# Kernel optimization log

Hardware: AMD Instinct MI355X
Metric: run time of the kernel (lower is better)

Reference implementation:

```python
import math
import jax, jax.numpy as jnp
import numpy as np

L, B, D, Z, H, N = 2048, 8, 1024, 128, 2048, 16
MAXPOS = 2048
LAPLACE_MU, LAPLACE_SIGMA = 0.707107, 0.282095


def setup_inputs() -> dict:
    key = jax.random.key(0)
    ks = jax.random.split(key, 14)
    def rn(k, shp, s=1.0):
        return jax.random.normal(k, shp, dtype=jnp.float32) * s
    return {
        "x": rn(ks[0], (L, B, D)),
        # MultiHeadEMA params (unidirectional: kernel_dim == D)
        "delta": rn(ks[1], (D, N, 1), 0.2),
        "alpha": rn(ks[2], (D, N, 1), 0.2),
        "beta_ema": rn(ks[3], (D, N, 1), 0.02) + 1.0,
        "gamma_ema": rn(ks[4], (D, N)),
        "omega": rn(ks[5], (D,)),
        # projections
        "v_w": rn(ks[6], (D, H), 0.02), "v_b": jnp.zeros((H,), jnp.float32),
        "mx_w": rn(ks[7], (D, Z + H + 2 * D), 0.02),
        "mx_b": jnp.zeros((Z + H + 2 * D,), jnp.float32),
        "h_w": rn(ks[8], (H, D), 0.02), "h_b": jnp.zeros((D,), jnp.float32),
        # q/k affine from shared z
        "qk_gamma": rn(ks[9], (2, Z), 0.1) + 1.0,
        "qk_beta": rn(ks[10], (2, Z), 0.1),
        # simple relative positional bias
        "rel_pos": rn(ks[11], (2 * MAXPOS - 1,), 0.02),
        # prenorm layernorm
        "ln_w": jnp.ones((D,), jnp.float32),
        "ln_b": jnp.zeros((D,), jnp.float32),
    }


def _laplace(x):
    x = (x - LAPLACE_MU) / (LAPLACE_SIGMA * math.sqrt(2.0))
    return 0.5 * (1.0 + jax.lax.erf(x))


def _layer_norm(x, w, b, eps=1e-5):
    mu = jnp.mean(x, axis=-1, keepdims=True)
    var = jnp.mean(jnp.square(x - mu), axis=-1, keepdims=True)
    return (x - mu) * jax.lax.rsqrt(var + eps) * w + b


def _rel_bias(rel_pos, seq_len):
    # SimpleRelativePositionalBias: Toeplitz (L, L) matrix from a 2L-1 vector
    bvec = rel_pos[MAXPOS - seq_len:MAXPOS + seq_len - 1]  # (2L-1,)
    t = jnp.pad(bvec, (0, seq_len))                         # (3L-1,)
    t = jnp.tile(t, seq_len)[:-seq_len].reshape(seq_len, 3 * seq_len - 2)
    r = (2 * seq_len - 1) // 2
    return t[:, r:t.shape[1] - r]                           # (L, L)


def _ema_conv(xn, delta, alpha, beta_ema, gamma_ema, omega, seq_len):
    # xn: (L, B, D) -> silu(EMA(xn) + xn * omega), via FFT convolution
    scale = 1.0 / math.sqrt(N)
    p = jax.nn.sigmoid(delta)                 # (D, N, 1)
    q = 1.0 - p * jax.nn.sigmoid(alpha)       # (D, N, 1)
    vander = jnp.arange(seq_len, dtype=jnp.float32)[None, None, :] * jnp.log(q)  # (D, N, L)
    kernel = jnp.einsum('dnl,dn->dl', p * beta_ema * jnp.exp(vander), gamma_ema * scale)  # (D, L)
    residual = xn * omega                     # (L, B, D)
    xt = jnp.transpose(xn, (1, 2, 0))         # (B, D, L)
    nfft = 2 * seq_len
    kf = jnp.fft.rfft(kernel, n=nfft)         # (D, L+1) complex
    xf = jnp.fft.rfft(xt, n=nfft)             # (B, D, L+1)
    out = jnp.fft.irfft(xf * kf, n=nfft)[..., :seq_len]  # (B, D, L)
    return jax.nn.silu(jnp.transpose(out, (2, 0, 1)) + residual)  # (L, B, D)


def reference(x, delta, alpha, beta_ema, gamma_ema, omega,
              v_w, v_b, mx_w, mx_b, h_w, h_b,
              qk_gamma, qk_beta, rel_pos, ln_w, ln_b):
    seq_len = x.shape[0]
    residual = x
    xn = _layer_norm(x, ln_w, ln_b)                       # prenorm
    v = jax.nn.silu(xn @ v_w + v_b)                        # (L, B, H)
    mx = _ema_conv(xn, delta, alpha, beta_ema, gamma_ema, omega, seq_len)  # (L, B, D)
    base = mx @ mx_w + mx_b                                # (L, B, D+Z+H+D)
    u = jax.nn.sigmoid(base[..., :D])                      # update gate (L, B, D)
    zr = jax.nn.silu(base[..., D:D + Z + H])
    hx = base[..., D + Z + H:]                             # (L, B, D)
    z = zr[..., :Z]                                        # (L, B, Z)
    r = zr[..., Z:]                                        # (L, B, H)
    zqk = z[..., None, :] * qk_gamma + qk_beta             # (L, B, 2, Z)
    q = jnp.transpose(zqk[..., 0, :], (1, 0, 2))           # (B, L, Z)
    k = jnp.transpose(zqk[..., 1, :], (1, 0, 2))           # (B, L, Z)
    vb = jnp.transpose(v, (1, 0, 2))                       # (B, L, H)
    bias = _rel_bias(rel_pos, seq_len)                     # (L, L)
    qk = jnp.einsum('blz,bmz->blm', q, k) / seq_len + bias # (B, L, L)
    attn = _laplace(qk)
    h = jnp.einsum('blm,bmh->blh', attn, vb)               # (B, L, H)
    h = jnp.transpose(h, (1, 0, 2))                        # (L, B, H)
    h = jax.nn.silu(hx + (h * r) @ h_w + h_b)              # (L, B, D)
    out = residual + u * (h - residual)
    return out
```

## Files before the change

kernel.cpp:

```cpp
#include <hip/hip_runtime.h>
#include <hip/hip_bf16.h>
#include <math.h>

typedef unsigned short u16;
typedef unsigned int   u32;
typedef __bf16 bf16x8_t __attribute__((ext_vector_type(8)));
typedef float  f32x4_t  __attribute__((ext_vector_type(4)));

#define DEVI static __device__ __forceinline__

DEVI float bf2f(u16 u){ union{u32 i; float f;} v; v.i = ((u32)u)<<16; return v.f; }
DEVI u16 f2bf(float f){ union{float f; u32 i;} v; v.f = f; u32 i = v.i; i += 0x7fffu + ((i>>16)&1u); return (u16)(i>>16); }
DEVI float sigm(float x){ return 1.0f/(1.0f + __expf(-x)); }
DEVI float silu_(float x){ return x * sigm(x); }

DEVI void gload16(const u16* gsrc, u16* lds){
  __builtin_amdgcn_global_load_lds(
      (const __attribute__((address_space(1))) unsigned int*)gsrc,
      (__attribute__((address_space(3))) unsigned int*)lds, 16, 0, 0);
}

constexpr int L_=2048, B_=8, D_=1024, Z_=128, H_=2048, N_=16;
constexpr int CH_=128, NC_=16;
constexpr int MXN_=4224;

__global__ __launch_bounds__(256) void k_ln(const float* __restrict__ x,
                                            const float* __restrict__ w,
                                            const float* __restrict__ b,
                                            u16* __restrict__ xn){
  int row = blockIdx.x, t = threadIdx.x;
  int l = row >> 3, bb = row & 7;
  const float4* xr = (const float4*)(x + (size_t)row*D_);
  float4 v = xr[t];
  float s  = v.x+v.y+v.z+v.w;
  float sq = v.x*v.x+v.y*v.y+v.z*v.z+v.w*v.w;
  #pragma unroll
  for (int m=1; m<64; m<<=1){ s += __shfl_xor(s, m); sq += __shfl_xor(sq, m); }
  __shared__ float ss[4], sv[4];
  int wv = t>>6;
  if ((t&63)==0){ ss[wv]=s; sv[wv]=sq; }
  __syncthreads();
  s = ss[0]+ss[1]+ss[2]+ss[3]; sq = sv[0]+sv[1]+sv[2]+sv[3];
  float mu = s*(1.0f/D_);
  float var = sq*(1.0f/D_) - mu*mu;
  float rs = rsqrtf(var + 1e-5f);
  float4 wv4 = ((const float4*)w)[t];
  float4 bv4 = ((const float4*)b)[t];
  u16 o0 = f2bf((v.x-mu)*rs*wv4.x+bv4.x);
  u16 o1 = f2bf((v.y-mu)*rs*wv4.y+bv4.y);
  u16 o2 = f2bf((v.z-mu)*rs*wv4.z+bv4.z);
  u16 o3 = f2bf((v.w-mu)*rs*wv4.w+bv4.w);
  *(uint2*)(xn + ((size_t)bb*L_ + l)*D_ + t*4) =
      make_uint2((u32)o0 | ((u32)o1<<16), (u32)o2 | ((u32)o3<<16));
}

__global__ __launch_bounds__(256) void k_tr(const float* __restrict__ in, int R, int C,
                                            u16* __restrict__ out){
  __shared__ u16 TT[32*33];
  int c0 = blockIdx.x*32, r0 = blockIdx.y*32;
  int t = threadIdx.x;
  int lr = t>>3, lc4 = (t&7)*4;
  float4 v = *(const float4*)&in[(size_t)(r0+lr)*C + c0 + lc4];
  TT[(lc4+0)*33 + lr] = f2bf(v.x);
  TT[(lc4+1)*33 + lr] = f2bf(v.y);
  TT[(lc4+2)*33 + lr] = f2bf(v.z);
  TT[(lc4+3)*33 + lr] = f2bf(v.w);
  __syncthreads();
  int orr = t>>3, oc4 = (t&7)*4;
  u16 a0 = TT[orr*33 + oc4+0], a1 = TT[orr*33 + oc4+1];
  u16 a2 = TT[orr*33 + oc4+2], a3 = TT[orr*33 + oc4+3];
  *(uint2*)&out[(size_t)(c0+orr)*R + r0 + oc4] =
      make_uint2((u32)a0 | ((u32)a1<<16), (u32)a2 | ((u32)a3<<16));
}

__global__ void k_ema_params(const float* __restrict__ delta, const float* __restrict__ alpha,
                             const float* __restrict__ beta,  const float* __restrict__ gamma,
                             float* __restrict__ qA, float* __restrict__ wcA, float* __restrict__ qPA){
  int i = blockIdx.x*256 + threadIdx.x;
  if (i >= D_*N_) return;
  float p = 1.0f/(1.0f + expf(-delta[i]));
  float q = 1.0f - p*(1.0f/(1.0f + expf(-alpha[i])));
  qA[i]  = q;
  wcA[i] = p*beta[i]*gamma[i]*0.25f;
  qPA[i] = powf(q, (float)CH_);
}

__global__ __launch_bounds__(256) void k_ema_a(const u16* __restrict__ xn,
                                               const float* __restrict__ qA,
                                               float* __restrict__ F){
  int d = blockIdx.x*256 + threadIdx.x;
  int b = blockIdx.y, c = blockIdx.z;
  float q[N_], s[N_];
  #pragma unroll
  for (int n=0;n<N_;n++){ q[n]=qA[d*N_+n]; s[n]=0.0f; }
  for (int t=0;t<CH_;t++){
    int l = c*CH_ + t;
    float x = bf2f(xn[((size_t)b*L_ + l)*D_ + d]);
    #pragma unroll
    for (int n=0;n<N_;n++) s[n] = q[n]*s[n] + x;
  }
  float* Fo = F + (((size_t)c*B_ + b)*D_ + d)*N_;
  #pragma unroll
  for (int n=0;n<N_;n++) Fo[n] = s[n];
}

__global__ __launch_bounds__(256) void k_ema_b(float* __restrict__ F,
                                               const float* __restrict__ qPA){
  int i = blockIdx.x*256 + threadIdx.x;
  int n = i & (N_-1);
  int d = (i>>4) & (D_-1);
  int b = i >> 14;
  float qP = qPA[d*N_+n];
  float S = 0.0f;
  for (int c=0;c<NC_;c++){
    size_t idx = (((size_t)c*B_ + b)*D_ + d)*N_ + n;
    float f = F[idx];
    F[idx] = S;
    S = qP*S + f;
  }
}

__global__ __launch_bounds__(256) void k_ema_c(const u16* __restrict__ xn,
                                               const float* __restrict__ qA,
                                               const float* __restrict__ wcA,
                                               const float* __restrict__ CY,
                                               const float* __restrict__ omega,
                                               u16* __restrict__ mx){
  int d = blockIdx.x*256 + threadIdx.x;
  int b = blockIdx.y, c = blockIdx.z;
  float q[N_], wc[N_], s[N_];
  const float* cy = CY + (((size_t)c*B_ + b)*D_ + d)*N_;
  #pragma unroll
  for (int n=0;n<N_;n++){ q[n]=qA[d*N_+n]; wc[n]=wcA[d*N_+n]; s[n]=cy[n]; }
  float om = omega[d];
  for (int t=0;t<CH_;t++){
    int l = c*CH_ + t;
    float x = bf2f(xn[((size_t)b*L_ + l)*D_ + d]);
    float acc = 0.0f;
    #pragma unroll
    for (int n=0;n<N_;n++){ s[n] = q[n]*s[n] + x; acc += wc[n]*s[n]; }
    mx[((size_t)b*L_ + l)*D_ + d] = f2bf(silu_(acc + x*om));
  }
}

#define STG(BUF, K0) do {                                                         \
    int _ab = (BUF)*24576;                                                        \
    _Pragma("unroll")                                                             \
    for (int it=0; it<4; ++it){                                                   \
      int idx = it*512 + tid; int r = idx>>3, ch = idx&7;                         \
      gload16(Ab + (size_t)(rowBase + r)*lda + (K0) + ((ch ^ (r&7))*8),           \
              &LDS[_ab + idx*8]);                                                 \
    }                                                                             \
    _Pragma("unroll")                                                             \
    for (int it=0; it<2; ++it){                                                   \
      int idx = it*512 + tid; int r = idx>>3, ch = idx&7;                         \
      gload16(Bb + (size_t)(colBase + r)*ldb + (K0) + ((ch ^ (r&7))*8),           \
              &LDS[_ab + 16384 + idx*8]);                                         \
    }                                                                             \
  } while(0)

#define CMP(BUF) do {                                                             \
    int _ab = (BUF)*24576;                                                        \
    _Pragma("unroll")                                                             \
    for (int ks=0; ks<2; ++ks){                                                   \
      bf16x8_t af[4], bfr[4];                                                     \
      int kfx = (ks*32 + lane4*8) ^ ((lane15&7)<<3);                              \
      _Pragma("unroll")                                                           \
      for (int m=0;m<4;m++)                                                       \
        af[m]  = *(const bf16x8_t*)&LDS[_ab + (wr*64 + m*16 + lane15)*64 + kfx];  \
      _Pragma("unroll")                                                           \
      for (int n=0;n<4;n++)                                                       \
        bfr[n] = *(const bf16x8_t*)&LDS[_ab + 16384 + (wc*64 + n*16 + lane15)*64 + kfx]; \
      __builtin_amdgcn_s_setprio(1);                                              \
      _Pragma("unroll")                                                           \
      for (int m=0;m<4;m++)                                                       \
        _Pragma("unroll")                                                         \
        for (int n=0;n<4;n++)                                                     \
          acc[m][n] = __builtin_amdgcn_mfma_f32_16x16x32_bf16(af[m], bfr[n], acc[m][n], 0,0,0); \
      __builtin_amdgcn_s_setprio(0);                                              \
    }                                                                             \
  } while(0)

template<int OP>
__global__ __launch_bounds__(512, 2) void k_g256(
    const u16* __restrict__ A, int lda, long aStr,
    const u16* __restrict__ Bm, int ldb, long bStr,
    int K,
    u16* __restrict__ C, int ldc, long cStr,
    const float* __restrict__ biasC, const float* __restrict__ biasR,
    const float* __restrict__ qkg, const float* __restrict__ qkb,
    u16* __restrict__ P0, u16* __restrict__ P1,
    u16* __restrict__ P2, u16* __restrict__ P3,
    const u16* __restrict__ RP0)
{
  __shared__ u16 LDS[73728];
  int zz = blockIdx.z;
  const u16* Ab = A + (size_t)zz*aStr;
  const u16* Bb = Bm + (size_t)zz*bStr;
  int rowBase = blockIdx.y*256;
  int colBase = blockIdx.x*128;
  int tid = threadIdx.x;
  int lane = tid & 63, wave = tid >> 6;
  int wr = wave >> 1, wc = wave & 1;
  int lane15 = lane & 15, lane4 = lane >> 4;

  f32x4_t acc[4][4];
  #pragma unroll
  for (int m=0;m<4;m++)
    #pragma unroll
    for (int n=0;n<4;n++) acc[m][n] = (f32x4_t){0.f,0.f,0.f,0.f};

  int nt = K >> 6;
  STG(0, 0);
  STG(1, 64);
  for (int t = 0; t < nt; ++t){
    int cb = t % 3;
    if (t + 1 < nt) { asm volatile("s_waitcnt vmcnt(6)" ::: "memory"); }
    else            { asm volatile("s_waitcnt vmcnt(0)" ::: "memory"); }
    __builtin_amdgcn_s_barrier();
    __builtin_amdgcn_sched_barrier(0);
    if (t + 2 < nt) STG((t+2)%3, (t+2)*64);
    CMP(cb);
  }

  u16* Cb  = C  ? C  + (size_t)zz*cStr : nullptr;
  u16* P0b = P0 ? P0 + (size_t)zz*((size_t)L_*D_) : nullptr;
  u16* P1b = P1 ? P1 + (size_t)zz*((size_t)L_*D_) : nullptr;
  u16* P2b = P2 ? P2 + (size_t)zz*((size_t)L_*Z_) : nullptr;
  u16* P3b = P3 ? P3 + (size_t)zz*((size_t)L_*Z_) : nullptr;
  const u16* RP0b = RP0 ? RP0 + (size_t)zz*((size_t)L_*H_) : nullptr;

  #pragma unroll
  for (int m=0;m<4;m++) {
    #pragma unroll
    for (int n=0;n<4;n++) {
      int col = colBase + wc*64 + n*16 + lane15;
      #pragma unroll
      for (int r2=0;r2<4;r2++) {
        int row = rowBase + wr*64 + m*16 + lane4*4 + r2;
        float v = acc[m][n][r2];
        if (OP == 0) {
          Cb[(size_t)row*ldc + col] = f2bf(silu_(v + biasR[row]));
        } else if (OP == 1) {
          v += biasC[col];
          if (col < 1024) {
            P0b[(size_t)row*1024 + col] = f2bf(sigm(v));
          } else if (col < 1152) {
            float s = silu_(v);
            int zi = col - 1024;
            P2b[(size_t)row*128 + zi] = f2bf(s*qkg[zi]     + qkb[zi]);
            P3b[(size_t)row*128 + zi] = f2bf(s*qkg[128+zi] + qkb[128+zi]);
          } else if (col < 3200) {
            Cb[(size_t)row*2048 + (col-1152)] = f2bf(silu_(v));
          } else {
            P1b[(size_t)row*1024 + (col-3200)] = f2bf(v);
          }
        } else {
          v *= bf2f(RP0b[(size_t)row*ldc + col]);
          Cb[(size_t)row*ldc + col] = f2bf(v);
        }
      }
    }
  }
}

template<int OP>
__global__ __launch_bounds__(256) void k_gemm(
    const u16* __restrict__ A, int lda, long aStr,
    const u16* __restrict__ Bm, int ldb, long bStr,
    int K,
    u16* __restrict__ C, int ldc, long cStr,
    const float* __restrict__ biasC,
    const float* __restrict__ relpos,
    const u16* __restrict__ RP0, const u16* __restrict__ RP1,
    const float* __restrict__ xin, float* __restrict__ outf, int bb)
{
  __shared__ u16 Al[8192];
  __shared__ u16 Bl[8192];
  int zz = blockIdx.z;
  const u16* Ab = A + (size_t)zz*aStr;
  const u16* Bb = Bm + (size_t)zz*bStr;
  int rowBase = blockIdx.y*128;
  int colBase = blockIdx.x*128;
  int tid = threadIdx.x;
  int lane = tid & 63, wave = tid >> 6;
  int wm = (wave>>1)*64, wn = (wave&1)*64;
  int lane15 = lane & 15, lane4 = lane >> 4;

  f32x4_t acc[4][4];
  #pragma unroll
  for (int i=0;i<4;i++)
    #pragma unroll
    for (int j=0;j<4;j++) acc[i][j] = (f32x4_t){0.f,0.f,0.f,0.f};

  for (int k0 = 0; k0 < K; k0 += 64) {
    #pragma unroll
    for (int it=0; it<4; ++it) {
      int c = it*256 + tid;
      gload16(Ab + (size_t)(rowBase + (c>>3))*lda + k0 + (c&7)*8, &Al[c*8]);
    }
    #pragma unroll
    for (int it=0; it<4; ++it) {
      int c = it*256 + tid;
      gload16(Bb + (size_t)(colBase + (c>>3))*ldb + k0 + (c&7)*8, &Bl[c*8]);
    }
    __syncthreads();
    #pragma unroll
    for (int kk=0; kk<2; ++kk) {
      bf16x8_t af[4], bfr[4];
      int kf = kk*32 + lane4*8;
      #pragma unroll
      for (int i=0;i<4;i++) af[i] = *(const bf16x8_t*)&Al[(wm + i*16 + lane15)*64 + kf];
      #pragma unroll
      for (int j=0;j<4;j++) bfr[j] = *(const bf16x8_t*)&Bl[(wn + j*16 + lane15)*64 + kf];
      #pragma unroll
      for (int i=0;i<4;i++)
        #pragma unroll
        for (int j=0;j<4;j++)
          acc[i][j] = __builtin_amdgcn_mfma_f32_16x16x32_bf16(af[i], bfr[j], acc[i][j], 0,0,0);
    }
    __syncthreads();
  }

  u16* Cb = C ? C + (size_t)zz*cStr : nullptr;
  const u16* RP0b = RP0 ? RP0 + (size_t)zz*((size_t)L_*D_) : nullptr;
  const u16* RP1b = RP1 ? RP1 + (size_t)zz*((size_t)L_*D_) : nullptr;
  int bglob = bb + zz;

  #pragma unroll
  for (int i=0;i<4;i++) {
    #pragma unroll
    for (int j=0;j<4;j++) {
      int col = colBase + wn + j*16 + lane15;
      #pragma unroll
      for (int r2=0;r2<4;r2++) {
        int row = rowBase + wm + i*16 + lane4*4 + r2;
        float v = acc[i][j][r2];
        if (OP == 2) {
          v = v*(1.0f/(float)L_) + relpos[2047 + col - row];
          v = 0.5f*(1.0f + erff((v - 0.707107f)*2.5066282746f));
          Cb[(size_t)row*ldc + col] = f2bf(v);
        } else {
          v += biasC[col];
          float hx = bf2f(RP0b[(size_t)row*1024 + col]);
          float hval = silu_(hx + v);
          size_t gi = ((size_t)row*B_ + bglob)*D_ + col;
          float xv = xin[gi];
          float uu = bf2f(RP1b[(size_t)row*1024 + col]);
          outf[gi] = xv + uu*(hval - xv);
        }
      }
    }
  }
}

extern "C" void kernel_launch(void* const* d_in, const int* in_sizes, int n_in,
                              void* d_out, int out_size, void* d_ws, size_t ws_size,
                              hipStream_t stream) {
  const float* x      = (const float*)d_in[0];
  const float* delta  = (const float*)d_in[1];
  const float* alpha  = (const float*)d_in[2];
  const float* betaE  = (const float*)d_in[3];
  const float* gammaE = (const float*)d_in[4];
  const float* omega  = (const float*)d_in[5];
  const float* v_w    = (const float*)d_in[6];
  const float* v_b    = (const float*)d_in[7];
  const float* mx_w   = (const float*)d_in[8];
  const float* mx_b   = (const float*)d_in[9];
  const float* h_w    = (const float*)d_in[10];
  const float* h_b    = (const float*)d_in[11];
  const float* qkg    = (const float*)d_in[12];
  const float* qkb    = (const float*)d_in[13];
  const float* relpos = (const float*)d_in[14];
  const float* ln_w   = (const float*)d_in[15];
  const float* ln_b   = (const float*)d_in[16];
  float* out = (float*)d_out;

  const size_t fixedB = 92733440ull;
  const size_t perNB  = 42991616ull;
  int NB = 8;
  while (NB > 1 && fixedB + (size_t)NB*perNB > ws_size) NB >>= 1;
  int NG = B_ / NB;

  char* ws = (char*)d_ws;
  size_t o = 0;
  auto alloc = [&](size_t sz){ size_t r = o; o += sz; return r; };
  u16* XN    = (u16*)(ws + alloc(33554432));
  u16* MX    = (u16*)(ws + alloc(33554432));
  u16* VWT   = (u16*)(ws + alloc(4194304));
  u16* MXWT  = (u16*)(ws + alloc((size_t)MXN_*D_*2));
  u16* HWT   = (u16*)(ws + alloc(4194304));
  float* EQ  = (float*)(ws + alloc(65536));
  float* EW  = (float*)(ws + alloc(65536));
  float* EP  = (float*)(ws + alloc(65536));
  float* Ff  = (float*)(ws + alloc(8388608));
  u16* VT    = (u16*)(ws + alloc((size_t)NB*8388608));
  u16* ATTN  = (u16*)(ws + alloc((size_t)NB*8388608));
  u16* Rb    = (u16*)(ws + alloc((size_t)NB*8388608));
  u16* HRb   = (u16*)(ws + alloc((size_t)NB*8388608));
  u16* Ub    = (u16*)(ws + alloc((size_t)NB*4194304));
  u16* HXb   = (u16*)(ws + alloc((size_t)NB*4194304));
  u16* Qb    = (u16*)(ws + alloc((size_t)NB*524288));
  u16* Kb    = (u16*)(ws + alloc((size_t)NB*524288));

  k_ln<<<L_*B_, 256, 0, stream>>>(x, ln_w, ln_b, XN);
  k_ema_params<<<(D_*N_+255)/256, 256, 0, stream>>>(delta, alpha, betaE, gammaE, EQ, EW, EP);
  k_ema_a<<<dim3(D_/256, B_, NC_), 256, 0, stream>>>(XN, EQ, Ff);
  k_ema_b<<<(B_*D_*N_)/256, 256, 0, stream>>>(Ff, EP);
  k_ema_c<<<dim3(D_/256, B_, NC_), 256, 0, stream>>>(XN, EQ, EW, Ff, omega, MX);
  k_tr<<<dim3(H_/32, D_/32), 256, 0, stream>>>(v_w, D_, H_, VWT);
  k_tr<<<dim3(MXN_/32, D_/32), 256, 0, stream>>>(mx_w, D_, MXN_, MXWT);
  k_tr<<<dim3(D_/32, H_/32), 256, 0, stream>>>(h_w, H_, D_, HWT);

  for (int g = 0; g < NG; ++g) {
    int b0 = g*NB;
    k_g256<0><<<dim3(L_/128, H_/256, NB), 512, 0, stream>>>(
        VWT, D_, 0L, XN + (size_t)b0*L_*D_, D_, (long)L_*D_, D_,
        VT, L_, (long)H_*L_,
        nullptr, v_b, nullptr, nullptr,
        nullptr, nullptr, nullptr, nullptr, nullptr);
    k_g256<1><<<dim3(MXN_/128, L_/256, NB), 512, 0, stream>>>(
        MX + (size_t)b0*L_*D_, D_, (long)L_*D_, MXWT, D_, 0L, D_,
        Rb, H_, (long)L_*H_,
        mx_b, nullptr, qkg, qkb,
        Ub, HXb, Qb, Kb, nullptr);
    k_gemm<2><<<dim3(L_/128, L_/128, NB), 256, 0, stream>>>(
        Qb, Z_, (long)L_*Z_, Kb, Z_, (long)L_*Z_, Z_,
        ATTN, L_, (long)L_*L_,
        nullptr, relpos, nullptr, nullptr, nullptr, nullptr, 0);
    k_g256<3><<<dim3(H_/128, L_/256, NB), 512, 0, stream>>>(
        ATTN, L_, (long)L_*L_, VT, L_, (long)H_*L_, L_,
        HRb, H_, (long)L_*H_,
        nullptr, nullptr, nullptr, nullptr,
        nullptr, nullptr, nullptr, nullptr, Rb);
    k_gemm<4><<<dim3(D_/128, L_/128, NB), 256, 0, stream>>>(
        HRb, H_, (long)L_*H_, HWT, H_, 0L, H_,
        nullptr, 0, 0L,
        h_b, nullptr, HXb, Ub, x, out, b0);
  }
}
```

Before: 859.2 us.

## Unify all GEMMs into one 128x128 double-buffered swizzled kernel

Replaces the two GEMM kernels with a single 256-thread kernel that uses 128x128 tiles. The old 256x128 kernel had 512 threads, a triple-buffered pipeline and no extra barrier per step; the old 128x128 kernel had no overlap between loads and MFMAs and no LDS swizzle. The new kernel keeps a two-buffer global_load_lds pipeline with an XOR swizzle, and adds a barrier before each refill, for all five GEMM stages. The aim is to give the attention-score and output-projection GEMMs prefetching and conflict-free LDS reads, and to raise occupancy with less shared memory per block. The cost is less operand reuse per block on the larger V, mx and attention-times-V GEMMs.

```diff
diff --git a/kernel.cpp b/kernel.cpp
--- a/kernel.cpp
+++ b/kernel.cpp
@@ -144,33 +144,33 @@
 }
 
 #define STG(BUF, K0) do {                                                         \
-    int _ab = (BUF)*24576;                                                        \
+    int _ab = (BUF)*16384;                                                        \
     _Pragma("unroll")                                                             \
     for (int it=0; it<4; ++it){                                                   \
-      int idx = it*512 + tid; int r = idx>>3, ch = idx&7;                         \
+      int idx = it*256 + tid; int r = idx>>3, ch = idx&7;                         \
       gload16(Ab + (size_t)(rowBase + r)*lda + (K0) + ((ch ^ (r&7))*8),           \
               &LDS[_ab + idx*8]);                                                 \
     }                                                                             \
     _Pragma("unroll")                                                             \
-    for (int it=0; it<2; ++it){                                                   \
-      int idx = it*512 + tid; int r = idx>>3, ch = idx&7;                         \
+    for (int it=0; it<4; ++it){                                                   \
+      int idx = it*256 + tid; int r = idx>>3, ch = idx&7;                         \
       gload16(Bb + (size_t)(colBase + r)*ldb + (K0) + ((ch ^ (r&7))*8),           \
-              &LDS[_ab + 16384 + idx*8]);                                         \
+              &LDS[_ab + 8192 + idx*8]);                                          \
     }                                                                             \
   } while(0)
 
 #define CMP(BUF) do {                                                             \
-    int _ab = (BUF)*24576;                                                        \
+    int _ab = (BUF)*16384;                                                        \
     _Pragma("unroll")                                                             \
     for (int ks=0; ks<2; ++ks){                                                   \
       bf16x8_t af[4], bfr[4];                                                     \
       int kfx = (ks*32 + lane4*8) ^ ((lane15&7)<<3);                              \
       _Pragma("unroll")                                                           \
       for (int m=0;m<4;m++)                                                       \
-        af[m]  = *(const bf16x8_t*)&LDS[_ab + (wr*64 + m*16 + lane15)*64 + kfx];  \
+        af[m]  = *(const bf16x8_t*)&LDS[_ab + (wm + m*16 + lane15)*64 + kfx];     \
       _Pragma("unroll")                                                           \
       for (int n=0;n<4;n++)                                                       \
-        bfr[n] = *(const bf16x8_t*)&LDS[_ab + 16384 + (wc*64 + n*16 + lane15)*64 + kfx]; \
+        bfr[n] = *(const bf16x8_t*)&LDS[_ab + 8192 + (wn + n*16 + lane15)*64 + kfx]; \
       __builtin_amdgcn_s_setprio(1);                                              \
       _Pragma("unroll")                                                           \
       for (int m=0;m<4;m++)                                                       \
@@ -182,26 +182,28 @@
   } while(0)
 
 template<int OP>
-__global__ __launch_bounds__(512, 2) void k_g256(
+__global__ __launch_bounds__(256) void k_gall(
     const u16* __restrict__ A, int lda, long aStr,
     const u16* __restrict__ Bm, int ldb, long bStr,
     int K,
     u16* __restrict__ C, int ldc, long cStr,
     const float* __restrict__ biasC, const float* __restrict__ biasR,
+    const float* __restrict__ relpos,
     const float* __restrict__ qkg, const float* __restrict__ qkb,
     u16* __restrict__ P0, u16* __restrict__ P1,
     u16* __restrict__ P2, u16* __restrict__ P3,
-    const u16* __restrict__ RP0)
+    const u16* __restrict__ RP0, const u16* __restrict__ RP1,
+    const float* __restrict__ xin, float* __restrict__ outf, int bb)
 {
-  __shared__ u16 LDS[73728];
+  __shared__ u16 LDS[32768];
   int zz = blockIdx.z;
   const u16* Ab = A + (size_t)zz*aStr;
   const u16* Bb = Bm + (size_t)zz*bStr;
-  int rowBase = blockIdx.y*256;
+  int rowBase = blockIdx.y*128;
   int colBase = blockIdx.x*128;
   int tid = threadIdx.x;
   int lane = tid & 63, wave = tid >> 6;
-  int wr = wave >> 1, wc = wave & 1;
+  int wm = (wave>>1)*64, wn = (wave&1)*64;
   int lane15 = lane & 15, lane4 = lane >> 4;
 
   f32x4_t acc[4][4];
@@ -214,13 +216,15 @@
   STG(0, 0);
   STG(1, 64);
   for (int t = 0; t < nt; ++t){
-    int cb = t % 3;
-    if (t + 1 < nt) { asm volatile("s_waitcnt vmcnt(6)" ::: "memory"); }
+    if (t + 1 < nt) { asm volatile("s_waitcnt vmcnt(8)" ::: "memory"); }
     else            { asm volatile("s_waitcnt vmcnt(0)" ::: "memory"); }
     __builtin_amdgcn_s_barrier();
     __builtin_amdgcn_sched_barrier(0);
-    if (t + 2 < nt) STG((t+2)%3, (t+2)*64);
-    CMP(cb);
+    CMP(t & 1);
+    if (t + 2 < nt) {
+      __builtin_amdgcn_s_barrier();
+      STG(t & 1, (t+2)*64);
+    }
   }
 
   u16* Cb  = C  ? C  + (size_t)zz*cStr : nullptr;
@@ -228,16 +232,18 @@
   u16* P1b = P1 ? P1 + (size_t)zz*((size_t)L_*D_) : nullptr;
   u16* P2b = P2 ? P2 + (size_t)zz*((size_t)L_*Z_) : nullptr;
   u16* P3b = P3 ? P3 + (size_t)zz*((size_t)L_*Z_) : nullptr;
-  const u16* RP0b = RP0 ? RP0 + (size_t)zz*((size_t)L_*H_) : nullptr;
+  const u16* RP0b = RP0 ? RP0 + (size_t)zz*(OP==3 ? (size_t)L_*H_ : (size_t)L_*D_) : nullptr;
+  const u16* RP1b = RP1 ? RP1 + (size_t)zz*((size_t)L_*D_) : nullptr;
+  int bglob = bb + zz;
 
   #pragma unroll
   for (int m=0;m<4;m++) {
     #pragma unroll
     for (int n=0;n<4;n++) {
-      int col = colBase + wc*64 + n*16 + lane15;
+      int col = colBase + wn + n*16 + lane15;
       #pragma unroll
       for (int r2=0;r2<4;r2++) {
-        int row = rowBase + wr*64 + m*16 + lane4*4 + r2;
+        int row = rowBase + wm + m*16 + lane4*4 + r2;
         float v = acc[m][n][r2];
         if (OP == 0) {
           Cb[(size_t)row*ldc + col] = f2bf(silu_(v + biasR[row]));
@@ -255,90 +261,12 @@
           } else {
             P1b[(size_t)row*1024 + (col-3200)] = f2bf(v);
           }
-        } else {
-          v *= bf2f(RP0b[(size_t)row*ldc + col]);
-          Cb[(size_t)row*ldc + col] = f2bf(v);
-        }
-      }
-    }
-  }
-}
-
-template<int OP>
-__global__ __launch_bounds__(256) void k_gemm(
-    const u16* __restrict__ A, int lda, long aStr,
-    const u16* __restrict__ Bm, int ldb, long bStr,
-    int K,
-    u16* __restrict__ C, int ldc, long cStr,
-    const float* __restrict__ biasC,
-    const float* __restrict__ relpos,
-    const u16* __restrict__ RP0, const u16* __restrict__ RP1,
-    const float* __restrict__ xin, float* __restrict__ outf, int bb)
-{
-  __shared__ u16 Al[8192];
-  __shared__ u16 Bl[8192];
-  int zz = blockIdx.z;
-  const u16* Ab = A + (size_t)zz*aStr;
-  const u16* Bb = Bm + (size_t)zz*bStr;
-  int rowBase = blockIdx.y*128;
-  int colBase = blockIdx.x*128;
-  int tid = threadIdx.x;
-  int lane = tid & 63, wave = tid >> 6;
-  int wm = (wave>>1)*64, wn = (wave&1)*64;
-  int lane15 = lane & 15, lane4 = lane >> 4;
-
-  f32x4_t acc[4][4];
-  #pragma unroll
-  for (int i=0;i<4;i++)
-    #pragma unroll
-    for (int j=0;j<4;j++) acc[i][j] = (f32x4_t){0.f,0.f,0.f,0.f};
-
-  for (int k0 = 0; k0 < K; k0 += 64) {
-    #pragma unroll
-    for (int it=0; it<4; ++it) {
-      int c = it*256 + tid;
-      gload16(Ab + (size_t)(rowBase + (c>>3))*lda + k0 + (c&7)*8, &Al[c*8]);
-    }
-    #pragma unroll
-    for (int it=0; it<4; ++it) {
-      int c = it*256 + tid;
-      gload16(Bb + (size_t)(colBase + (c>>3))*ldb + k0 + (c&7)*8, &Bl[c*8]);
-    }
-    __syncthreads();
-    #pragma unroll
-    for (int kk=0; kk<2; ++kk) {
-      bf16x8_t af[4], bfr[4];
-      int kf = kk*32 + lane4*8;
-      #pragma unroll
-      for (int i=0;i<4;i++) af[i] = *(const bf16x8_t*)&Al[(wm + i*16 + lane15)*64 + kf];
-      #pragma unroll
-      for (int j=0;j<4;j++) bfr[j] = *(const bf16x8_t*)&Bl[(wn + j*16 + lane15)*64 + kf];
-      #pragma unroll
-      for (int i=0;i<4;i++)
-        #pragma unroll
-        for (int j=0;j<4;j++)
-          acc[i][j] = __builtin_amdgcn_mfma_f32_16x16x32_bf16(af[i], bfr[j], acc[i][j], 0,0,0);
-    }
-    __syncthreads();
-  }
-
-  u16* Cb = C ? C + (size_t)zz*cStr : nullptr;
-  const u16* RP0b = RP0 ? RP0 + (size_t)zz*((size_t)L_*D_) : nullptr;
-  const u16* RP1b = RP1 ? RP1 + (size_t)zz*((size_t)L_*D_) : nullptr;
-  int bglob = bb + zz;
-
-  #pragma unroll
-  for (int i=0;i<4;i++) {
-    #pragma unroll
-    for (int j=0;j<4;j++) {
-      int col = colBase + wn + j*16 + lane15;
-      #pragma unroll
-      for (int r2=0;r2<4;r2++) {
-        int row = rowBase + wm + i*16 + lane4*4 + r2;
-        float v = acc[i][j][r2];
-        if (OP == 2) {
+        } else if (OP == 2) {
           v = v*(1.0f/(float)L_) + relpos[2047 + col - row];
           v = 0.5f*(1.0f + erff((v - 0.707107f)*2.5066282746f));
+          Cb[(size_t)row*ldc + col] = f2bf(v);
+        } else if (OP == 3) {
+          v *= bf2f(RP0b[(size_t)row*ldc + col]);
           Cb[(size_t)row*ldc + col] = f2bf(v);
         } else {
           v += biasC[col];
@@ -414,28 +342,35 @@
 
   for (int g = 0; g < NG; ++g) {
     int b0 = g*NB;
-    k_g256<0><<<dim3(L_/128, H_/256, NB), 512, 0, stream>>>(
+    k_gall<0><<<dim3(L_/128, H_/128, NB), 256, 0, stream>>>(
         VWT, D_, 0L, XN + (size_t)b0*L_*D_, D_, (long)L_*D_, D_,
         VT, L_, (long)H_*L_,
-        nullptr, v_b, nullptr, nullptr,
-        nullptr, nullptr, nullptr, nullptr, nullptr);
-    k_g256<1><<<dim3(MXN_/128, L_/256, NB), 512, 0, stream>>>(
+        nullptr, v_b, nullptr, nullptr, nullptr,
+        nullptr, nullptr, nullptr, nullptr,
+        nullptr, nullptr, nullptr, nullptr, 0);
+    k_gall<1><<<dim3(MXN_/128, L_/128, NB), 256, 0, stream>>>(
         MX + (size_t)b0*L_*D_, D_, (long)L_*D_, MXWT, D_, 0L, D_,
         Rb, H_, (long)L_*H_,
-        mx_b, nullptr, qkg, qkb,
-        Ub, HXb, Qb, Kb, nullptr);
-    k_gemm<2><<<dim3(L_/128, L_/128, NB), 256, 0, stream>>>(
+        mx_b, nullptr, nullptr, qkg, qkb,
+        Ub, HXb, Qb, Kb,
+        nullptr, nullptr, nullptr, nullptr, 0);
+    k_gall<2><<<dim3(L_/128, L_/128, NB), 256, 0, stream>>>(
         Qb, Z_, (long)L_*Z_, Kb, Z_, (long)L_*Z_, Z_,
         ATTN, L_, (long)L_*L_,
-        nullptr, relpos, nullptr, nullptr, nullptr, nullptr, 0);
-    k_g256<3><<<dim3(H_/128, L_/256, NB), 512, 0, stream>>>(
+        nullptr, nullptr, relpos, nullptr, nullptr,
+        nullptr, nullptr, nullptr, nullptr,
+        nullptr, nullptr, nullptr, nullptr, 0);
+    k_gall<3><<<dim3(H_/128, L_/128, NB), 256, 0, stream>>>(
         ATTN, L_, (long)L_*L_, VT, L_, (long)H_*L_, L_,
         HRb, H_, (long)L_*H_,
+        nullptr, nullptr, nullptr, nullptr, nullptr,
         nullptr, nullptr, nullptr, nullptr,
-        nullptr, nullptr, nullptr, nullptr, Rb);
-    k_gemm<4><<<dim3(D_/128, L_/128, NB), 256, 0, stream>>>(
+        Rb, nullptr, nullptr, nullptr, 0);
+    k_gall<4><<<dim3(D_/128, L_/128, NB), 256, 0, stream>>>(
         HRb, H_, (long)L_*H_, HWT, H_, 0L, H_,
         nullptr, 0, 0L,
-        h_b, nullptr, HXb, Ub, x, out, b0);
-  }
-}
+        h_b, nullptr, nullptr, nullptr, nullptr,
+        nullptr, nullptr, nullptr, nullptr,
+        HXb, Ub, x, out, b0);
+  }
+}
```

Result: faster. 795.1 us (-7.5%).
